# Kernel tuning notes

Measured on AMD Instinct MI355X. Metric: run time of the kernel, lower is better.

## Reference

```python
import jax, jax.numpy as jnp
import numpy as np
from jax.ops import segment_sum, segment_max

N, E, G = 20000, 100000, 16
TILE, EMB, HID, OUT, FEAT, HEADS = 32, 128, 256, 512, 512, 8
SLOPE = 0.2


def setup_inputs() -> dict:
    key = jax.random.key(0)
    ks = jax.random.split(key, 20)
    def gn(k, shape, fan_in):
        return jax.random.normal(k, shape, jnp.float32) * (1.0 / np.sqrt(fan_in))
    return {
        "x": jax.random.normal(ks[0], (N, TILE), jnp.float32),
        "edge_index": jax.random.randint(ks[1], (2, E), 0, N, jnp.int32),
        "batch": jnp.sort(jax.random.randint(ks[2], (N,), 0, G, jnp.int32)),
        "W0": gn(ks[3], (TILE, EMB), TILE), "b0": jnp.zeros((EMB,), jnp.float32),
        "W1": gn(ks[4], (EMB, HEADS * HID), EMB),
        "a1s": gn(ks[5], (HEADS, HID), HID), "a1d": gn(ks[6], (HEADS, HID), HID),
        "b1": jnp.zeros((HEADS * HID,), jnp.float32),
        "W2": gn(ks[7], (HEADS * HID, HEADS * HID), HEADS * HID),
        "a2s": gn(ks[8], (HEADS, HID), HID), "a2d": gn(ks[9], (HEADS, HID), HID),
        "b2": jnp.zeros((HEADS * HID,), jnp.float32),
        "W3": gn(ks[10], (HEADS * HID, OUT), HEADS * HID),
        "a3s": gn(ks[11], (1, OUT), OUT), "a3d": gn(ks[12], (1, OUT), OUT),
        "b3": jnp.zeros((OUT,), jnp.float32),
        "Wf": gn(ks[13], (OUT, FEAT), OUT), "bf": jnp.zeros((FEAT,), jnp.float32),
    }


def gat_conv(x, src, dst, W, a_s, a_d, b, heads, ch, n):
    # PyG GATConv: linear, per-edge additive attention, segment softmax over dst, scatter-add
    h = (x @ W).reshape(n, heads, ch)                       # [N,H,C]
    e_src = jnp.einsum("nhc,hc->nh", h, a_s)                 # [N,H]
    e_dst = jnp.einsum("nhc,hc->nh", h, a_d)
    e = jax.nn.leaky_relu(e_src[src] + e_dst[dst], SLOPE)    # [E,H]
    m = segment_max(e, dst, num_segments=n)                  # [N,H]
    m = jax.lax.stop_gradient(jnp.where(jnp.isfinite(m), m, 0.0))
    ex = jnp.exp(e - m[dst])
    den = segment_sum(ex, dst, num_segments=n)
    alpha = ex / (den[dst] + 1e-16)                          # [E,H]
    out = segment_sum(h[src] * alpha[..., None], dst, num_segments=n)  # [N,H,C]
    return out.reshape(n, heads * ch) + b


def reference(x, edge_index, batch, W0, b0, W1, a1s, a1d, b1, W2, a2s, a2d, b2,
              W3, a3s, a3d, b3, Wf, bf):
    loop = jnp.arange(N, dtype=edge_index.dtype)             # PyG adds self-loops by default
    src = jnp.concatenate([edge_index[0], loop])
    dst = jnp.concatenate([edge_index[1], loop])
    h = jax.nn.leaky_relu(x @ W0 + b0, SLOPE)
    h = jax.nn.leaky_relu(gat_conv(h, src, dst, W1, a1s, a1d, b1, HEADS, HID, N), SLOPE)
    h = jax.nn.leaky_relu(gat_conv(h, src, dst, W2, a2s, a2d, b2, HEADS, HID, N), SLOPE)
    h = jax.nn.leaky_relu(gat_conv(h, src, dst, W3, a3s, a3d, b3, 1, OUT, N), SLOPE)
    sums = segment_sum(h, batch, num_segments=G)             # global_mean_pool
    cnt = segment_sum(jnp.ones((N,), h.dtype), batch, num_segments=G)
    mean = sums / jnp.maximum(cnt, 1.0)[:, None]
    return jax.nn.leaky_relu(mean @ Wf + bf, SLOPE)
```

## Files before the change

kernel.cpp:

```cpp
#include <hip/hip_runtime.h>
#include <hip/hip_bf16.h>

#define N_NODES 20000
#define N_EDGES 100000
#define ET (N_EDGES + N_NODES)
#define G_GRAPHS 16
#define SLOPE 0.2f

using short8  = __attribute__((ext_vector_type(8))) short;
using floatx4 = __attribute__((ext_vector_type(4))) float;

__device__ __forceinline__ float lrelu(float x) { return x > 0.f ? x : SLOPE * x; }

__device__ __forceinline__ float b2f(unsigned short u) {
    union { unsigned int i; float f; } v; v.i = ((unsigned int)u) << 16; return v.f;
}
__device__ __forceinline__ unsigned short f2b(float f) {
    union { float f; unsigned int i; } v; v.f = f;
    unsigned int i = v.i;
    return (unsigned short)((i + 0x7fffu + ((i >> 16) & 1u)) >> 16);
}

__device__ __forceinline__ void gld16(const void* g, void* l) {
    __builtin_amdgcn_global_load_lds((const __attribute__((address_space(1))) void*)g,
                                     (__attribute__((address_space(3))) void*)l, 16, 0, 0);
}

__device__ int dev_lower_bound(const int* a, int n, int key) {
    int lo = 0, hi = n;
    while (lo < hi) { int mid = (lo + hi) >> 1; if (a[mid] < key) lo = mid + 1; else hi = mid; }
    return lo;
}

__global__ void zero_kernel(int* __restrict__ p, int n) {
    int i = blockIdx.x * blockDim.x + threadIdx.x;
    if (i < n) p[i] = 0;
}

__global__ void count_kernel(const int* __restrict__ ei, int* __restrict__ counts) {
    int e = blockIdx.x * blockDim.x + threadIdx.x;
    if (e >= ET) return;
    int dst = (e < N_EDGES) ? ei[N_EDGES + e] : (e - N_EDGES);
    atomicAdd(&counts[dst], 1);
}

__global__ void scan_kernel(const int* __restrict__ counts, int* __restrict__ row_ptr) {
    __shared__ int sums[256];
    int t = threadIdx.x;
    const int CH = (N_NODES + 255) / 256;
    int base = t * CH;
    int s = 0;
    for (int i = 0; i < CH; i++) { int idx = base + i; if (idx < N_NODES) s += counts[idx]; }
    sums[t] = s;
    __syncthreads();
    for (int off = 1; off < 256; off <<= 1) {
        int v = (t >= off) ? sums[t - off] : 0;
        __syncthreads();
        sums[t] += v;
        __syncthreads();
    }
    int run = (t == 0) ? 0 : sums[t - 1];
    for (int i = 0; i < CH; i++) {
        int idx = base + i;
        if (idx < N_NODES) { row_ptr[idx] = run; run += counts[idx]; }
    }
    if (t == 255) row_ptr[N_NODES] = run;
}

__global__ void fill_kernel(const int* __restrict__ ei, const int* __restrict__ row_ptr,
                            int* __restrict__ fill_cnt, int* __restrict__ col) {
    int e = blockIdx.x * blockDim.x + threadIdx.x;
    if (e >= ET) return;
    int src, dst;
    if (e < N_EDGES) { src = ei[e]; dst = ei[N_EDGES + e]; }
    else             { src = dst = e - N_EDGES; }
    int pos = atomicAdd(&fill_cnt[dst], 1);
    col[row_ptr[dst] + pos] = src;
}

__global__ void transpose_kernel(const float* __restrict__ W, unsigned short* __restrict__ Wt,
                                 int K, int N) {
    __shared__ float tile[32][33];
    int bn = blockIdx.x * 32, bk = blockIdx.y * 32;
    int tx = threadIdx.x & 31, ty = threadIdx.x >> 5;
#pragma unroll
    for (int p = 0; p < 32; p += 8)
        tile[ty + p][tx] = W[(size_t)(bk + ty + p) * N + bn + tx];
    __syncthreads();
#pragma unroll
    for (int p = 0; p < 32; p += 8)
        Wt[(size_t)(bn + ty + p) * K + bk + tx] = f2b(tile[tx][ty + p]);
}

__global__ void gemm0_kernel(const float* __restrict__ x, const float* __restrict__ W0,
                             const float* __restrict__ b0, unsigned short* __restrict__ h0) {
    __shared__ float xr[32];
    int n = blockIdx.x, t = threadIdx.x;
    if (t < 32) xr[t] = x[n * 32 + t];
    __syncthreads();
    float acc = 0.f;
#pragma unroll
    for (int k = 0; k < 32; k++) acc += xr[k] * W0[k * 128 + t];
    h0[(size_t)n * 128 + t] = f2b(lrelu(acc + b0[t]));
}

__global__ __launch_bounds__(256) void gemm_mfma(const unsigned short* __restrict__ A,
                                                 const unsigned short* __restrict__ Bt,
                                                 unsigned short* __restrict__ C,
                                                 int M, int N, int K) {
    __shared__ __align__(16) unsigned short As[128][32];
    __shared__ __align__(16) unsigned short Bs[128][32];
    int t = threadIdx.x;
    int w = t >> 6, l = t & 63;
    int r0 = blockIdx.y * 128, c0 = blockIdx.x * 128;
    int wr = (w >> 1) * 64, wc = (w & 1) * 64;
    int lrow = l >> 2;
    int gcb  = (l & 3) ^ ((l >> 3) & 3);
    int m16 = l & 15, qb = l >> 4;
    int sw  = (m16 >> 1) & 3;
    int roff = ((qb ^ sw) * 8);
    floatx4 acc[4][4] = {};

    for (int k0 = 0; k0 < K; k0 += 32) {
        __syncthreads();
#pragma unroll
        for (int q = 0; q < 2; q++) {
            int row = w * 32 + q * 16 + lrow;
            int ga = min(r0 + row, M - 1);
            gld16(A + (size_t)ga * K + k0 + gcb * 8, &As[w * 32 + q * 16][0]);
            gld16(Bt + (size_t)(c0 + row) * K + k0 + gcb * 8, &Bs[w * 32 + q * 16][0]);
        }
        __syncthreads();
        short8 af[4], bfr[4];
#pragma unroll
        for (int i = 0; i < 4; i++) af[i] = *(const short8*)&As[wr + i * 16 + m16][roff];
#pragma unroll
        for (int j = 0; j < 4; j++) bfr[j] = *(const short8*)&Bs[wc + j * 16 + m16][roff];
#pragma unroll
        for (int i = 0; i < 4; i++)
#pragma unroll
            for (int j = 0; j < 4; j++)
                acc[i][j] = __builtin_amdgcn_mfma_f32_16x16x32_bf16(af[i], bfr[j], acc[i][j], 0, 0, 0);
    }
    int quad = l >> 4;
#pragma unroll
    for (int i = 0; i < 4; i++)
#pragma unroll
        for (int j = 0; j < 4; j++)
#pragma unroll
            for (int reg = 0; reg < 4; reg++) {
                int r = r0 + wr + i * 16 + quad * 4 + reg;
                int c = c0 + wc + j * 16 + m16;
                if (r < M) C[(size_t)r * N + c] = f2b(acc[i][j][reg]);
            }
}

__global__ void att8_kernel(const unsigned short* __restrict__ h, const float* __restrict__ a_s,
                            const float* __restrict__ a_d, float* __restrict__ es,
                            float* __restrict__ ed) {
    int n = blockIdx.x, t = threadIdx.x;
    int hd = t >> 5, l = t & 31;
    const unsigned short* hr = h + (size_t)n * 2048 + hd * 256 + l * 8;
    const float* as_ = a_s + hd * 256 + l * 8;
    const float* ad_ = a_d + hd * 256 + l * 8;
    uint4 u = *(const uint4*)hr;
    float v[8] = { b2f((unsigned short)(u.x & 0xffff)), b2f((unsigned short)(u.x >> 16)),
                   b2f((unsigned short)(u.y & 0xffff)), b2f((unsigned short)(u.y >> 16)),
                   b2f((unsigned short)(u.z & 0xffff)), b2f((unsigned short)(u.z >> 16)),
                   b2f((unsigned short)(u.w & 0xffff)), b2f((unsigned short)(u.w >> 16)) };
    float s1 = 0.f, s2 = 0.f;
#pragma unroll
    for (int j = 0; j < 8; j++) { s1 += v[j] * as_[j]; s2 += v[j] * ad_[j]; }
    for (int m = 16; m >= 1; m >>= 1) { s1 += __shfl_xor(s1, m); s2 += __shfl_xor(s2, m); }
    if (l == 0) { es[n * 8 + hd] = s1; ed[n * 8 + hd] = s2; }
}

__global__ void att1_kernel(const unsigned short* __restrict__ h, const float* __restrict__ a_s,
                            const float* __restrict__ a_d, float* __restrict__ es,
                            float* __restrict__ ed) {
    int n = blockIdx.x, l = threadIdx.x;
    const unsigned short* hr = h + (size_t)n * 512 + l * 8;
    const float* as_ = a_s + l * 8;
    const float* ad_ = a_d + l * 8;
    uint4 u = *(const uint4*)hr;
    float v[8] = { b2f((unsigned short)(u.x & 0xffff)), b2f((unsigned short)(u.x >> 16)),
                   b2f((unsigned short)(u.y & 0xffff)), b2f((unsigned short)(u.y >> 16)),
                   b2f((unsigned short)(u.z & 0xffff)), b2f((unsigned short)(u.z >> 16)),
                   b2f((unsigned short)(u.w & 0xffff)), b2f((unsigned short)(u.w >> 16)) };
    float s1 = 0.f, s2 = 0.f;
#pragma unroll
    for (int j = 0; j < 8; j++) { s1 += v[j] * as_[j]; s2 += v[j] * ad_[j]; }
    for (int m = 32; m >= 1; m >>= 1) { s1 += __shfl_xor(s1, m); s2 += __shfl_xor(s2, m); }
    if (l == 0) { es[n] = s1; ed[n] = s2; }
}

template <int H, int C>
__global__ __launch_bounds__(256) void agg_fused(const unsigned short* __restrict__ hmid,
                                                 const float* __restrict__ es,
                                                 const float* __restrict__ ed,
                                                 const int* __restrict__ row_ptr,
                                                 const int* __restrict__ col,
                                                 const float* __restrict__ bias,
                                                 unsigned short* __restrict__ out) {
    constexpr int HC = H * C;
    constexpr int PT = HC / 256;
    constexpr int LH = (H == 8) ? 3 : 0;
    __shared__ float sm_ed[H], sm_m[H], sm_den[H];
    __shared__ float wpart[4 * H];
    __shared__ float sm_alpha[32][H];
    __shared__ int scol[32];
    int v = blockIdx.x, t = threadIdx.x;
    int rs = row_ptr[v], deg = row_ptr[v + 1] - rs;
    if (t < H) sm_ed[t] = ed[v * H + t];
    __syncthreads();
    int h = t & (H - 1);
    int w = t >> 6, l = t & 63;
    float edv = sm_ed[h];
    float lmax = -1e30f;
    for (int e = t >> LH; e < deg; e += 256 / H) {
        int s = col[rs + e];
        lmax = fmaxf(lmax, lrelu(es[s * H + h] + edv));
    }
#pragma unroll
    for (int m = H; m < 64; m <<= 1) lmax = fmaxf(lmax, __shfl_xor(lmax, m));
    if (l < H) wpart[w * H + l] = lmax;
    __syncthreads();
    if (t < H)
        sm_m[t] = fmaxf(fmaxf(wpart[t], wpart[H + t]), fmaxf(wpart[2 * H + t], wpart[3 * H + t]));
    __syncthreads();
    float mh = sm_m[h];
    float lsum = 0.f;
    for (int e = t >> LH; e < deg; e += 256 / H) {
        int s = col[rs + e];
        lsum += __expf(lrelu(es[s * H + h] + edv) - mh);
    }
#pragma unroll
    for (int m = H; m < 64; m <<= 1) lsum += __shfl_xor(lsum, m);
    if (l < H) wpart[w * H + l] = lsum;
    __syncthreads();
    if (t < H) sm_den[t] = wpart[t] + wpart[H + t] + wpart[2 * H + t] + wpart[3 * H + t];
    int j0 = t * PT;
    int hd = j0 / C;
    float acc[PT] = {};
    for (int cs = 0; cs < deg; cs += 32) {
        int cn = min(32, deg - cs);
        __syncthreads();
        if (t < cn) scol[t] = col[rs + cs + t];
        __syncthreads();
        if (t < cn * H) {
            int ce = t / H, hh = t % H;
            float lg = lrelu(es[scol[ce] * H + hh] + sm_ed[hh]);
            sm_alpha[ce][hh] = __expf(lg - sm_m[hh]) / (sm_den[hh] + 1e-16f);
        }
        __syncthreads();
        for (int ce = 0; ce < cn; ce++) {
            float a = sm_alpha[ce][hd];
            const unsigned short* hr = hmid + (size_t)scol[ce] * HC + j0;
            if constexpr (PT == 8) {
                uint4 u = *(const uint4*)hr;
                acc[0] += a * b2f((unsigned short)(u.x & 0xffff));
                acc[1] += a * b2f((unsigned short)(u.x >> 16));
                acc[2] += a * b2f((unsigned short)(u.y & 0xffff));
                acc[3] += a * b2f((unsigned short)(u.y >> 16));
                acc[4] += a * b2f((unsigned short)(u.z & 0xffff));
                acc[5] += a * b2f((unsigned short)(u.z >> 16));
                acc[6] += a * b2f((unsigned short)(u.w & 0xffff));
                acc[7] += a * b2f((unsigned short)(u.w >> 16));
            } else {
                unsigned int u = *(const unsigned int*)hr;
                acc[0] += a * b2f((unsigned short)(u & 0xffff));
                acc[1] += a * b2f((unsigned short)(u >> 16));
            }
        }
    }
    unsigned short o[PT];
#pragma unroll
    for (int i = 0; i < PT; i++) o[i] = f2b(lrelu(acc[i] + bias[j0 + i]));
    if constexpr (PT == 8) {
        *(uint4*)&out[(size_t)v * HC + j0] = *(const uint4*)o;
    } else {
        *(unsigned int*)&out[(size_t)v * HC + j0] = *(const unsigned int*)o;
    }
}

__global__ void pool_kernel(const unsigned short* __restrict__ h3, const int* __restrict__ batch,
                            float* __restrict__ msum) {
    int b0 = blockIdx.x * 128, t = threadIdx.x;
    int nend = min(b0 + 128, N_NODES);
    int curg = batch[b0];
    float s0 = 0.f, s1 = 0.f;
    for (int n = b0; n < nend; n++) {
        int g = batch[n];
        if (g != curg) {
            atomicAdd(&msum[curg * 512 + t * 2], s0);
            atomicAdd(&msum[curg * 512 + t * 2 + 1], s1);
            s0 = s1 = 0.f; curg = g;
        }
        unsigned int u = *(const unsigned int*)&h3[(size_t)n * 512 + t * 2];
        s0 += b2f((unsigned short)(u & 0xffff));
        s1 += b2f((unsigned short)(u >> 16));
    }
    atomicAdd(&msum[curg * 512 + t * 2], s0);
    atomicAdd(&msum[curg * 512 + t * 2 + 1], s1);
}

__global__ void final_kernel(const float* __restrict__ msum, const int* __restrict__ batch,
                             const float* __restrict__ Wf, const float* __restrict__ bf,
                             float* __restrict__ out) {
    int g = blockIdx.x, t = threadIdx.x;
    __shared__ float mr[512];
    __shared__ float sinv;
    if (t == 0) {
        int st = dev_lower_bound(batch, N_NODES, g);
        int en = dev_lower_bound(batch, N_NODES, g + 1);
        sinv = 1.f / fmaxf((float)(en - st), 1.f);
    }
    __syncthreads();
    for (int c = t; c < 512; c += 256) mr[c] = msum[g * 512 + c] * sinv;
    __syncthreads();
    for (int j = t; j < 512; j += 256) {
        float s = 0.f;
        for (int k = 0; k < 512; k++) s += mr[k] * Wf[k * 512 + j];
        out[g * 512 + j] = lrelu(s + bf[j]);
    }
}

extern "C" void kernel_launch(void* const* d_in, const int* in_sizes, int n_in,
                              void* d_out, int out_size, void* d_ws, size_t ws_size,
                              hipStream_t stream) {
    const float* x   = (const float*)d_in[0];
    const int*   ei  = (const int*)d_in[1];
    const int*   bat = (const int*)d_in[2];
    const float* W0  = (const float*)d_in[3];
    const float* b0  = (const float*)d_in[4];
    const float* W1  = (const float*)d_in[5];
    const float* a1s = (const float*)d_in[6];
    const float* a1d = (const float*)d_in[7];
    const float* b1  = (const float*)d_in[8];
    const float* W2  = (const float*)d_in[9];
    const float* a2s = (const float*)d_in[10];
    const float* a2d = (const float*)d_in[11];
    const float* b2  = (const float*)d_in[12];
    const float* W3  = (const float*)d_in[13];
    const float* a3s = (const float*)d_in[14];
    const float* a3d = (const float*)d_in[15];
    const float* b3  = (const float*)d_in[16];
    const float* Wf  = (const float*)d_in[17];
    const float* bf  = (const float*)d_in[18];
    float* out = (float*)d_out;

    char* p = (char*)d_ws;
    unsigned short* bufA = (unsigned short*)p; p += (size_t)N_NODES * 2048 * 2;
    unsigned short* bufB = (unsigned short*)p; p += (size_t)N_NODES * 2048 * 2;
    unsigned short* h0   = (unsigned short*)p; p += (size_t)N_NODES * 128 * 2;
    unsigned short* W1t  = (unsigned short*)p; p += (size_t)2048 * 128 * 2;
    unsigned short* W2t  = (unsigned short*)p; p += (size_t)2048 * 2048 * 2;
    unsigned short* W3t  = (unsigned short*)p; p += (size_t)512 * 2048 * 2;
    float* es   = (float*)p; p += (size_t)N_NODES * 8 * 4;
    float* ed   = (float*)p; p += (size_t)N_NODES * 8 * 4;
    float* msum = (float*)p; p += 16 * 512 * 4;
    int* counts  = (int*)p; p += (size_t)N_NODES * 4;
    int* row_ptr = (int*)p; p += (size_t)(N_NODES + 1) * 4;
    int* col     = (int*)p; p += (size_t)ET * 4;

    zero_kernel<<<(N_NODES + 255) / 256, 256, 0, stream>>>(counts, N_NODES);
    count_kernel<<<(ET + 255) / 256, 256, 0, stream>>>(ei, counts);
    scan_kernel<<<1, 256, 0, stream>>>(counts, row_ptr);
    zero_kernel<<<(N_NODES + 255) / 256, 256, 0, stream>>>(counts, N_NODES);
    fill_kernel<<<(ET + 255) / 256, 256, 0, stream>>>(ei, row_ptr, counts, col);

    transpose_kernel<<<dim3(2048 / 32, 128 / 32), 256, 0, stream>>>(W1, W1t, 128, 2048);
    transpose_kernel<<<dim3(2048 / 32, 2048 / 32), 256, 0, stream>>>(W2, W2t, 2048, 2048);
    transpose_kernel<<<dim3(512 / 32, 2048 / 32), 256, 0, stream>>>(W3, W3t, 2048, 512);

    gemm0_kernel<<<N_NODES, 128, 0, stream>>>(x, W0, b0, h0);

    dim3 g12(2048 / 128, (N_NODES + 127) / 128);
    dim3 g3(512 / 128, (N_NODES + 127) / 128);

    gemm_mfma<<<g12, 256, 0, stream>>>(h0, W1t, bufB, N_NODES, 2048, 128);
    att8_kernel<<<N_NODES, 256, 0, stream>>>(bufB, a1s, a1d, es, ed);
    agg_fused<8, 256><<<N_NODES, 256, 0, stream>>>(bufB, es, ed, row_ptr, col, b1, bufA);

    gemm_mfma<<<g12, 256, 0, stream>>>(bufA, W2t, bufB, N_NODES, 2048, 2048);
    att8_kernel<<<N_NODES, 256, 0, stream>>>(bufB, a2s, a2d, es, ed);
    agg_fused<8, 256><<<N_NODES, 256, 0, stream>>>(bufB, es, ed, row_ptr, col, b2, bufA);

    gemm_mfma<<<g3, 256, 0, stream>>>(bufA, W3t, bufB, N_NODES, 512, 2048);
    att1_kernel<<<N_NODES, 64, 0, stream>>>(bufB, a3s, a3d, es, ed);
    agg_fused<1, 512><<<N_NODES, 256, 0, stream>>>(bufB, es, ed, row_ptr, col, b3, bufA);

    zero_kernel<<<(16 * 512 + 255) / 256, 256, 0, stream>>>((int*)msum, 16 * 512);
    pool_kernel<<<(N_NODES + 127) / 128, 256, 0, stream>>>(bufA, bat, msum);
    final_kernel<<<G_GRAPHS, 256, 0, stream>>>(msum, bat, Wf, bf, out);
}
```

Measured before the change: 836.4 us.

## Fuse softmax normalization into aggregation and vectorize GEMM output stores

The aggregation kernel no longer runs separate max and denominator passes over each node's edges. It computes exp of the raw logits once per chunk, accumulates the denominator alongside the weighted sum, and divides at the end. Dropping the max subtraction removes two edge passes and several block barriers, but exp can overflow when logits are large. The GEMM swaps its MFMA operands so each lane holds four consecutive output columns, which lets it write one ushort4 store instead of scalar strided stores.

```diff
diff --git a/kernel.cpp b/kernel.cpp
--- a/kernel.cpp
+++ b/kernel.cpp
@@ -140,19 +140,22 @@
         for (int i = 0; i < 4; i++)
 #pragma unroll
             for (int j = 0; j < 4; j++)
-                acc[i][j] = __builtin_amdgcn_mfma_f32_16x16x32_bf16(af[i], bfr[j], acc[i][j], 0, 0, 0);
+                acc[i][j] = __builtin_amdgcn_mfma_f32_16x16x32_bf16(bfr[j], af[i], acc[i][j], 0, 0, 0);
     }
     int quad = l >> 4;
 #pragma unroll
-    for (int i = 0; i < 4; i++)
-#pragma unroll
-        for (int j = 0; j < 4; j++)
-#pragma unroll
-            for (int reg = 0; reg < 4; reg++) {
-                int r = r0 + wr + i * 16 + quad * 4 + reg;
-                int c = c0 + wc + j * 16 + m16;
-                if (r < M) C[(size_t)r * N + c] = f2b(acc[i][j][reg]);
+    for (int i = 0; i < 4; i++) {
+        int r = r0 + wr + i * 16 + m16;
+        if (r < M) {
+#pragma unroll
+            for (int j = 0; j < 4; j++) {
+                int c = c0 + wc + j * 16 + quad * 4;
+                ushort4 o = make_ushort4(f2b(acc[i][j][0]), f2b(acc[i][j][1]),
+                                         f2b(acc[i][j][2]), f2b(acc[i][j][3]));
+                *(ushort4*)&C[(size_t)r * N + c] = o;
             }
+        }
+    }
 }
 
 __global__ void att8_kernel(const unsigned short* __restrict__ h, const float* __restrict__ a_s,
@@ -204,44 +207,16 @@
                                                  unsigned short* __restrict__ out) {
     constexpr int HC = H * C;
     constexpr int PT = HC / 256;
-    constexpr int LH = (H == 8) ? 3 : 0;
-    __shared__ float sm_ed[H], sm_m[H], sm_den[H];
-    __shared__ float wpart[4 * H];
-    __shared__ float sm_alpha[32][H];
+    __shared__ float sm_ed[H];
+    __shared__ float sm_ex[32][H];
     __shared__ int scol[32];
     int v = blockIdx.x, t = threadIdx.x;
     int rs = row_ptr[v], deg = row_ptr[v + 1] - rs;
     if (t < H) sm_ed[t] = ed[v * H + t];
-    __syncthreads();
-    int h = t & (H - 1);
-    int w = t >> 6, l = t & 63;
-    float edv = sm_ed[h];
-    float lmax = -1e30f;
-    for (int e = t >> LH; e < deg; e += 256 / H) {
-        int s = col[rs + e];
-        lmax = fmaxf(lmax, lrelu(es[s * H + h] + edv));
-    }
-#pragma unroll
-    for (int m = H; m < 64; m <<= 1) lmax = fmaxf(lmax, __shfl_xor(lmax, m));
-    if (l < H) wpart[w * H + l] = lmax;
-    __syncthreads();
-    if (t < H)
-        sm_m[t] = fmaxf(fmaxf(wpart[t], wpart[H + t]), fmaxf(wpart[2 * H + t], wpart[3 * H + t]));
-    __syncthreads();
-    float mh = sm_m[h];
-    float lsum = 0.f;
-    for (int e = t >> LH; e < deg; e += 256 / H) {
-        int s = col[rs + e];
-        lsum += __expf(lrelu(es[s * H + h] + edv) - mh);
-    }
-#pragma unroll
-    for (int m = H; m < 64; m <<= 1) lsum += __shfl_xor(lsum, m);
-    if (l < H) wpart[w * H + l] = lsum;
-    __syncthreads();
-    if (t < H) sm_den[t] = wpart[t] + wpart[H + t] + wpart[2 * H + t] + wpart[3 * H + t];
     int j0 = t * PT;
     int hd = j0 / C;
     float acc[PT] = {};
+    float den = 0.f;
     for (int cs = 0; cs < deg; cs += 32) {
         int cn = min(32, deg - cs);
         __syncthreads();
@@ -249,12 +224,12 @@
         __syncthreads();
         if (t < cn * H) {
             int ce = t / H, hh = t % H;
-            float lg = lrelu(es[scol[ce] * H + hh] + sm_ed[hh]);
-            sm_alpha[ce][hh] = __expf(lg - sm_m[hh]) / (sm_den[hh] + 1e-16f);
+            sm_ex[ce][hh] = __expf(lrelu(es[scol[ce] * H + hh] + sm_ed[hh]));
         }
         __syncthreads();
         for (int ce = 0; ce < cn; ce++) {
-            float a = sm_alpha[ce][hd];
+            float a = sm_ex[ce][hd];
+            den += a;
             const unsigned short* hr = hmid + (size_t)scol[ce] * HC + j0;
             if constexpr (PT == 8) {
                 uint4 u = *(const uint4*)hr;
@@ -273,9 +248,10 @@
             }
         }
     }
+    float inv = 1.f / (den + 1e-16f);
     unsigned short o[PT];
 #pragma unroll
-    for (int i = 0; i < PT; i++) o[i] = f2b(lrelu(acc[i] + bias[j0 + i]));
+    for (int i = 0; i < PT; i++) o[i] = f2b(lrelu(acc[i] * inv + bias[j0 + i]));
     if constexpr (PT == 8) {
         *(uint4*)&out[(size_t)v * HC + j0] = *(const uint4*)o;
     } else {
```

Result: no change. 823.7 us (-1.5%).
